# Optimization experiments

Hardware: AMD Instinct MI355X
Metric: run time of the kernel (lower is better)

The kernel has to match this reference:

```python
import jax, jax.numpy as jnp
import numpy as np

D = 2048      # hidden_size
H = 16        # num_attention_heads
KVH = 4       # num_key_value_heads
HD = 128      # head_dim
E = 32        # num_experts
TOPK = 8      # num_experts_per_tok
F = 768       # moe_intermediate_size
EPS = 1e-6
THETA = 1000000.0
B, S = 2, 1024


def setup_inputs() -> dict:
    key = jax.random.key(0)
    ks = jax.random.split(key, 16)
    sc = lambda *shape: 1.0 / np.sqrt(shape[-2] if len(shape) > 1 else shape[0])
    return {
        "hidden_states": jax.random.normal(ks[0], (B, S, D), jnp.float32),
        "attention_mask": jnp.ones((B, S), jnp.bool_),
        "input_ln_scale": jnp.ones((D,), jnp.float32),
        "post_ln_scale": jnp.ones((D,), jnp.float32),
        "q_w": jax.random.normal(ks[1], (D, H * HD), jnp.float32) * sc(D, H * HD),
        "k_w": jax.random.normal(ks[2], (D, KVH * HD), jnp.float32) * sc(D, KVH * HD),
        "v_w": jax.random.normal(ks[3], (D, KVH * HD), jnp.float32) * sc(D, KVH * HD),
        "o_w": jax.random.normal(ks[4], (H * HD, D), jnp.float32) * sc(H * HD, D),
        "q_norm_scale": jnp.ones((HD,), jnp.float32),
        "k_norm_scale": jnp.ones((HD,), jnp.float32),
        "gate_w": jax.random.normal(ks[5], (D, E), jnp.float32) * sc(D, E),
        "gate_proj": jax.random.normal(ks[6], (E, D, F), jnp.float32) * sc(E, D, F),
        "up_proj": jax.random.normal(ks[7], (E, D, F), jnp.float32) * sc(E, D, F),
        "down_proj": jax.random.normal(ks[8], (E, F, D), jnp.float32) * sc(E, F, D),
    }


def _rms(x, scale):
    return x * jax.lax.rsqrt(jnp.mean(x * x, axis=-1, keepdims=True) + EPS) * scale


def _rope(x):
    # x: [B, S, h, HD]
    half = HD // 2
    inv_freq = 1.0 / (THETA ** (jnp.arange(0, half, dtype=jnp.float32) / half))
    freqs = jnp.arange(x.shape[1], dtype=jnp.float32)[:, None] * inv_freq  # [S, HD/2]
    cos = jnp.concatenate([jnp.cos(freqs)] * 2, axis=-1)[None, :, None, :]
    sin = jnp.concatenate([jnp.sin(freqs)] * 2, axis=-1)[None, :, None, :]
    rot = jnp.concatenate([-x[..., half:], x[..., :half]], axis=-1)
    return x * cos + rot * sin


def _forward(hidden_states, attention_mask, input_ln_scale, post_ln_scale,
             q_w, k_w, v_w, o_w, q_norm_scale, k_norm_scale,
             gate_w, gate_proj, up_proj, down_proj):
    b, s, _ = hidden_states.shape
    residual = hidden_states
    h = _rms(hidden_states, input_ln_scale)

    # ---- Qwen3 attention (GQA + per-head RMSNorm + RoPE, causal) ----
    q = _rms((h @ q_w).reshape(b, s, H, HD), q_norm_scale)
    k = _rms((h @ k_w).reshape(b, s, KVH, HD), k_norm_scale)
    v = (h @ v_w).reshape(b, s, KVH, HD)
    q, k = _rope(q), _rope(k)
    rep = H // KVH
    k = jnp.repeat(k, rep, axis=2)  # [B,S,H,HD]
    v = jnp.repeat(v, rep, axis=2)
    scores = jnp.einsum('bqhd,bkhd->bhqk', q, k) * (HD ** -0.5)
    causal = jnp.tril(jnp.ones((s, s), jnp.bool_))
    mask = causal[None, None] & attention_mask[:, None, None, :]
    scores = jnp.where(mask, scores, jnp.finfo(scores.dtype).min)
    attn = jax.nn.softmax(scores, axis=-1)
    ctx = jnp.einsum('bhqk,bkhd->bqhd', attn, v).reshape(b, s, H * HD)
    h = residual + ctx @ o_w

    # ---- MoE block ----
    residual = h
    x = _rms(h, post_ln_scale).reshape(-1, D)  # [N, D]
    router_logits = x @ gate_w                 # [N, E]
    routing_weights, selected = jax.lax.top_k(router_logits, k=TOPK)
    routing_weights = jax.nn.softmax(routing_weights, axis=-1)
    sel_flat = jnp.ravel(selected)                     # [N*K]
    x_exp = jnp.repeat(x, TOPK, axis=0)                # [N*K, D]
    sort_idx = jnp.argsort(sel_flat)
    unsort_idx = jnp.argsort(sort_idx)
    x_sorted = x_exp[sort_idx]
    group_sizes = jnp.bincount(sel_flat, length=E)
    gate_out = jax.lax.ragged_dot(x_sorted, gate_proj, group_sizes)
    up_out = jax.lax.ragged_dot(x_sorted, up_proj, group_sizes)
    activated = jax.nn.silu(gate_out) * up_out
    down_out = jax.lax.ragged_dot(activated, down_proj, group_sizes)
    unsorted = down_out[unsort_idx].reshape(-1, TOPK, D)
    moe_out = (unsorted * routing_weights[..., None]).sum(axis=1).reshape(b, s, D)
    return residual + moe_out


def reference(hidden_states, attention_mask, input_ln_scale, post_ln_scale,
              q_w, k_w, v_w, o_w, q_norm_scale, k_norm_scale,
              gate_w, gate_proj, up_proj, down_proj):
    return _forward(hidden_states, attention_mask, input_ln_scale, post_ln_scale,
                    q_w, k_w, v_w, o_w, q_norm_scale, k_norm_scale,
                    gate_w, gate_proj, up_proj, down_proj)
```

## Files before the change

kernel.cpp:

```cpp
#include <hip/hip_runtime.h>
#include <hip/hip_bf16.h>

#define D_ 2048
#define H_ 16
#define KVH_ 4
#define HD_ 128
#define E_ 32
#define TOPK_ 8
#define F_ 768
#define NB_ 2
#define SS_ 1024
#define NT_ 2048
#define NPAIR_ 16384

typedef __attribute__((ext_vector_type(8))) short short8;
typedef __attribute__((ext_vector_type(4))) float floatx4;
typedef __attribute__((ext_vector_type(4))) unsigned int uintx4;
typedef __attribute__((ext_vector_type(4))) unsigned short ushortx4;

__device__ __forceinline__ unsigned short f2bf(float f) {
  union { float f; unsigned u; } v; v.f = f;
  unsigned r = v.u + 0x7FFFu + ((v.u >> 16) & 1u);
  return (unsigned short)(r >> 16);
}
__device__ __forceinline__ float bf2f(unsigned short h) {
  union { unsigned u; float f; } v; v.u = ((unsigned)h) << 16;
  return v.f;
}
__device__ __forceinline__ void split2(float v, unsigned short& hi, unsigned short& lo) {
  unsigned short h = f2bf(v);
  hi = h;
  lo = f2bf(v - bf2f(h));
}
__device__ __forceinline__ void gload16(const unsigned short* g, unsigned short* l) {
  __builtin_amdgcn_global_load_lds(
      (const __attribute__((address_space(1))) unsigned int*)g,
      (__attribute__((address_space(3))) unsigned int*)l, 16, 0, 0);
}

__global__ __launch_bounds__(256) void tconv_kernel(const float* __restrict__ src,
                                                    unsigned short* __restrict__ dst,
                                                    int R, int C) {
  size_t off = (size_t)blockIdx.z * R * C;
  src += off; dst += off;
  __shared__ float t[32][33];
  int c0 = blockIdx.x * 32, r0 = blockIdx.y * 32;
  int row = threadIdx.x >> 3, c4 = (threadIdx.x & 7) * 4;
  float4 v = *(const float4*)(src + (size_t)(r0 + row) * C + c0 + c4);
  t[row][c4 + 0] = v.x; t[row][c4 + 1] = v.y; t[row][c4 + 2] = v.z; t[row][c4 + 3] = v.w;
  __syncthreads();
  ushortx4 o = { f2bf(t[c4 + 0][row]), f2bf(t[c4 + 1][row]),
                 f2bf(t[c4 + 2][row]), f2bf(t[c4 + 3][row]) };
  *(ushortx4*)(dst + (size_t)(c0 + row) * R + r0 + c4) = o;
}

__global__ __launch_bounds__(256) void tsplit_kernel(const float* __restrict__ src,
                                                     unsigned short* __restrict__ dhi,
                                                     unsigned short* __restrict__ dlo,
                                                     int R, int C) {
  __shared__ float t[32][33];
  int c0 = blockIdx.x * 32, r0 = blockIdx.y * 32;
  int row = threadIdx.x >> 3, c4 = (threadIdx.x & 7) * 4;
  float4 v = *(const float4*)(src + (size_t)(r0 + row) * C + c0 + c4);
  t[row][c4 + 0] = v.x; t[row][c4 + 1] = v.y; t[row][c4 + 2] = v.z; t[row][c4 + 3] = v.w;
  __syncthreads();
  ushortx4 oh, ol;
  #pragma unroll
  for (int i = 0; i < 4; ++i) {
    unsigned short hi, lo;
    split2(t[c4 + i][row], hi, lo);
    oh[i] = hi; ol[i] = lo;
  }
  size_t didx = (size_t)(c0 + row) * R + r0 + c4;
  *(ushortx4*)(dhi + didx) = oh;
  *(ushortx4*)(dlo + didx) = ol;
}

template<int MODE>
__global__ __launch_bounds__(256) void rms_kernel(const float* __restrict__ in,
                                                  const float* __restrict__ sc,
                                                  float* __restrict__ outf,
                                                  unsigned short* __restrict__ o1,
                                                  unsigned short* __restrict__ o2) {
  __shared__ float red[4];
  int row = blockIdx.x, tid = threadIdx.x;
  const float4* x4 = (const float4*)(in + (size_t)row * D_);
  float4 a = x4[tid], b = x4[tid + 256];
  float ss = a.x*a.x + a.y*a.y + a.z*a.z + a.w*a.w
           + b.x*b.x + b.y*b.y + b.z*b.z + b.w*b.w;
  #pragma unroll
  for (int off = 1; off < 64; off <<= 1) ss += __shfl_xor(ss, off);
  if ((tid & 63) == 0) red[tid >> 6] = ss;
  __syncthreads();
  float r = rsqrtf((red[0] + red[1] + red[2] + red[3]) * (1.0f / D_) + 1e-6f);
  const float4* s4 = (const float4*)sc;
  float4 sa = s4[tid], sb = s4[tid + 256];
  float va[8] = { a.x*r*sa.x, a.y*r*sa.y, a.z*r*sa.z, a.w*r*sa.w,
                  b.x*r*sb.x, b.y*r*sb.y, b.z*r*sb.z, b.w*r*sb.w };
  if (MODE == 0) {
    ushortx4 h0, l0, h1, l1;
    #pragma unroll
    for (int i = 0; i < 4; ++i) { unsigned short h, l; split2(va[i], h, l); h0[i] = h; l0[i] = l; }
    #pragma unroll
    for (int i = 0; i < 4; ++i) { unsigned short h, l; split2(va[4 + i], h, l); h1[i] = h; l1[i] = l; }
    *(ushortx4*)(o1 + (size_t)row * D_ + tid * 4) = h0;
    *(ushortx4*)(o2 + (size_t)row * D_ + tid * 4) = l0;
    *(ushortx4*)(o1 + (size_t)row * D_ + 1024 + tid * 4) = h1;
    *(ushortx4*)(o2 + (size_t)row * D_ + 1024 + tid * 4) = l1;
  } else {
    *(float4*)(outf + (size_t)row * D_ + tid * 4) = make_float4(va[0], va[1], va[2], va[3]);
    *(float4*)(outf + (size_t)row * D_ + 1024 + tid * 4) = make_float4(va[4], va[5], va[6], va[7]);
    ushortx4 h0 = { f2bf(va[0]), f2bf(va[1]), f2bf(va[2]), f2bf(va[3]) };
    ushortx4 h1 = { f2bf(va[4]), f2bf(va[5]), f2bf(va[6]), f2bf(va[7]) };
    *(ushortx4*)(o1 + (size_t)row * D_ + tid * 4) = h0;
    *(ushortx4*)(o1 + (size_t)row * D_ + 1024 + tid * 4) = h1;
  }
}

template<int EPI>
__global__ __launch_bounds__(256) void gemm_bb(const unsigned short* __restrict__ Ahi,
                                               const unsigned short* __restrict__ Alo,
                                               const unsigned short* __restrict__ Bhi,
                                               const unsigned short* __restrict__ Blo,
                                               const float* __restrict__ res,
                                               float* __restrict__ out,
                                               int M, int Nn, int K) {
  __shared__ unsigned short Ah[64 * 72], Al[64 * 72], Bh[64 * 72], Bl[64 * 72];
  int tid = threadIdx.x, l = tid & 63, wid = tid >> 6;
  int lr = l & 15, lk = (l >> 4) * 8;
  int m0 = blockIdx.y * 64, n0 = blockIdx.x * 64;
  int wr = (wid >> 1) * 32, wc = (wid & 1) * 32;
  int srow = tid >> 3, sch = (tid & 7) * 8;
  size_t aoff[2], boff[2];
  int loff[2];
  #pragma unroll
  for (int i = 0; i < 2; ++i) {
    aoff[i] = (size_t)(m0 + i * 32 + srow) * K + sch;
    boff[i] = (size_t)(n0 + i * 32 + srow) * K + sch;
    loff[i] = (i * 32 + srow) * 72 + sch;
  }
  floatx4 acc[2][2];
  #pragma unroll
  for (int i = 0; i < 2; ++i)
    #pragma unroll
    for (int j = 0; j < 2; ++j) acc[i][j] = (floatx4){0.f, 0.f, 0.f, 0.f};
  for (int k0 = 0; k0 < K; k0 += 64) {
    uintx4 vah[2], val[2], vbh[2], vbl[2];
    #pragma unroll
    for (int i = 0; i < 2; ++i) {
      vah[i] = *(const uintx4*)(Ahi + aoff[i] + k0);
      val[i] = *(const uintx4*)(Alo + aoff[i] + k0);
      vbh[i] = *(const uintx4*)(Bhi + boff[i] + k0);
      vbl[i] = *(const uintx4*)(Blo + boff[i] + k0);
    }
    __syncthreads();
    #pragma unroll
    for (int i = 0; i < 2; ++i) {
      *(uintx4*)&Ah[loff[i]] = vah[i];
      *(uintx4*)&Al[loff[i]] = val[i];
      *(uintx4*)&Bh[loff[i]] = vbh[i];
      *(uintx4*)&Bl[loff[i]] = vbl[i];
    }
    __syncthreads();
    #pragma unroll
    for (int ks = 0; ks < 2; ++ks) {
      short8 ah[2], al_[2], bh[2], bl_[2];
      #pragma unroll
      for (int i = 0; i < 2; ++i) {
        ah[i]  = *(const short8*)&Ah[(wr + i * 16 + lr) * 72 + ks * 32 + lk];
        al_[i] = *(const short8*)&Al[(wr + i * 16 + lr) * 72 + ks * 32 + lk];
        bh[i]  = *(const short8*)&Bh[(wc + i * 16 + lr) * 72 + ks * 32 + lk];
        bl_[i] = *(const short8*)&Bl[(wc + i * 16 + lr) * 72 + ks * 32 + lk];
      }
      #pragma unroll
      for (int i = 0; i < 2; ++i)
        #pragma unroll
        for (int j = 0; j < 2; ++j) {
          acc[i][j] = __builtin_amdgcn_mfma_f32_16x16x32_bf16(ah[i], bh[j], acc[i][j], 0, 0, 0);
          acc[i][j] = __builtin_amdgcn_mfma_f32_16x16x32_bf16(ah[i], bl_[j], acc[i][j], 0, 0, 0);
          acc[i][j] = __builtin_amdgcn_mfma_f32_16x16x32_bf16(al_[i], bh[j], acc[i][j], 0, 0, 0);
        }
    }
  }
  int rq = (l >> 4) * 4;
  #pragma unroll
  for (int i = 0; i < 2; ++i)
    #pragma unroll
    for (int j = 0; j < 2; ++j)
      #pragma unroll
      for (int r = 0; r < 4; ++r) {
        size_t idx = (size_t)(m0 + wr + i * 16 + rq + r) * Nn + (n0 + wc + j * 16 + lr);
        float v = acc[i][j][r];
        if (EPI == 1) v += res[idx];
        out[idx] = v;
      }
}

template<int EPI>
__global__ __launch_bounds__(256) void gemm_bb128g(const unsigned short* __restrict__ Ahi,
                                                   const unsigned short* __restrict__ Alo,
                                                   const unsigned short* __restrict__ Bhi,
                                                   const unsigned short* __restrict__ Blo,
                                                   const float* __restrict__ res,
                                                   float* __restrict__ out,
                                                   int M, int Nn, int K) {
  int g = blockIdx.x;
  int nwg = gridDim.x;
  int per = nwg >> 3;
  int sw = (g & 7) * per + (g >> 3);
  int my = M >> 7;
  int xt = sw / my, yt = sw - xt * my;
  int m0 = yt * 128, n0 = xt * 128;
  __shared__ unsigned short Ah[2][128 * 32], Al[2][128 * 32];
  __shared__ unsigned short Bh[2][128 * 32], Bl[2][128 * 32];
  int tid = threadIdx.x, l = tid & 63, wid = tid >> 6;
  int lr = l & 15, lk = (l >> 4) * 8;
  int wr = (wid >> 1) * 64, wc = (wid & 1) * 64;
  int srl = l >> 2;
  int sch = ((l & 3) ^ (srl & 3)) * 8;
  size_t aoffs[2], boffs[2];
  int ldo[2];
  #pragma unroll
  for (int i = 0; i < 2; ++i) {
    int r = wid * 32 + i * 16 + srl;
    aoffs[i] = (size_t)(m0 + r) * K + sch;
    boffs[i] = (size_t)(n0 + r) * K + sch;
    ldo[i] = (wid * 32 + i * 16) * 32;
  }
  floatx4 acc[4][4];
  #pragma unroll
  for (int i = 0; i < 4; ++i)
    #pragma unroll
    for (int j = 0; j < 4; ++j) acc[i][j] = (floatx4){0.f, 0.f, 0.f, 0.f};

  auto stage = [&](int sel, int k0) {
    #pragma unroll
    for (int i = 0; i < 2; ++i) {
      gload16(Ahi + aoffs[i] + k0, &Ah[sel][ldo[i]]);
      gload16(Alo + aoffs[i] + k0, &Al[sel][ldo[i]]);
      gload16(Bhi + boffs[i] + k0, &Bh[sel][ldo[i]]);
      gload16(Blo + boffs[i] + k0, &Bl[sel][ldo[i]]);
    }
  };

  int rsw = ((l >> 4) ^ (lr & 3)) << 3;
  stage(0, 0);
  asm volatile("s_waitcnt vmcnt(0)" ::: "memory");
  __syncthreads();
  for (int k0 = 0; k0 < K; k0 += 32) {
    int cur = (k0 >> 5) & 1;
    if (k0 + 32 < K) stage(cur ^ 1, k0 + 32);
    short8 ah[4], al_[4];
    #pragma unroll
    for (int i = 0; i < 4; ++i) {
      int ao = (wr + i * 16 + lr) * 32 + rsw;
      ah[i]  = *(const short8*)&Ah[cur][ao];
      al_[i] = *(const short8*)&Al[cur][ao];
    }
    #pragma unroll
    for (int j = 0; j < 4; ++j) {
      int bo = (wc + j * 16 + lr) * 32 + rsw;
      short8 bh  = *(const short8*)&Bh[cur][bo];
      short8 bl_ = *(const short8*)&Bl[cur][bo];
      #pragma unroll
      for (int i = 0; i < 4; ++i) {
        acc[i][j] = __builtin_amdgcn_mfma_f32_16x16x32_bf16(ah[i], bh, acc[i][j], 0, 0, 0);
        acc[i][j] = __builtin_amdgcn_mfma_f32_16x16x32_bf16(ah[i], bl_, acc[i][j], 0, 0, 0);
        acc[i][j] = __builtin_amdgcn_mfma_f32_16x16x32_bf16(al_[i], bh, acc[i][j], 0, 0, 0);
      }
    }
    asm volatile("s_waitcnt vmcnt(0)" ::: "memory");
    __syncthreads();
  }
  int rq = (l >> 4) * 4;
  #pragma unroll
  for (int i = 0; i < 4; ++i)
    #pragma unroll
    for (int j = 0; j < 4; ++j)
      #pragma unroll
      for (int r = 0; r < 4; ++r) {
        size_t idx = (size_t)(m0 + wr + i * 16 + rq + r) * Nn + (n0 + wc + j * 16 + lr);
        float v = acc[i][j][r];
        if (EPI == 1) v += res[idx];
        out[idx] = v;
      }
}

__global__ __launch_bounds__(256) void qknorm_rope_kernel(const float* __restrict__ qb,
                                                          const float* __restrict__ kb,
                                                          const float* __restrict__ qs,
                                                          const float* __restrict__ ks,
                                                          unsigned short* __restrict__ qhi,
                                                          unsigned short* __restrict__ qlo,
                                                          unsigned short* __restrict__ khi,
                                                          unsigned short* __restrict__ klo) {
  int gw = blockIdx.x * 4 + (threadIdx.x >> 6);
  int l = threadIdx.x & 63;
  const float* ptr; const float* sc; unsigned short *dhi, *dlo; int t;
  size_t orow;
  if (gw < NT_ * H_) { ptr = qb + (size_t)gw * HD_; sc = qs; dhi = qhi; dlo = qlo; orow = (size_t)gw * HD_; t = gw >> 4; }
  else { int r = gw - NT_ * H_; ptr = kb + (size_t)r * HD_; sc = ks; dhi = khi; dlo = klo; orow = (size_t)r * HD_; t = r >> 2; }
  int pos = t & (SS_ - 1);
  float2 x = *(const float2*)(ptr + 2 * l);
  float p2 = x.x * x.x + x.y * x.y;
  #pragma unroll
  for (int off = 1; off < 64; off <<= 1) p2 += __shfl_xor(p2, off);
  float rms = rsqrtf(p2 * (1.0f / HD_) + 1e-6f);
  float nx = x.x * rms * sc[2 * l];
  float ny = x.y * rms * sc[2 * l + 1];
  int j0 = (2 * l) & 63;
  float ang0 = pos * __expf(-(float)j0 * (13.815510557964274f / 64.0f));
  float ang1 = pos * __expf(-(float)(j0 + 1) * (13.815510557964274f / 64.0f));
  float s0, c0, s1, c1;
  sincosf(ang0, &s0, &c0);
  sincosf(ang1, &s1, &c1);
  float ox = __shfl_xor(nx, 32);
  float oy = __shfl_xor(ny, 32);
  float r0, r1;
  if (l < 32) { r0 = nx * c0 - ox * s0; r1 = ny * c1 - oy * s1; }
  else        { r0 = nx * c0 + ox * s0; r1 = ny * c1 + oy * s1; }
  unsigned short h0, l0, h1, l1;
  split2(r0, h0, l0);
  split2(r1, h1, l1);
  *(unsigned*)(dhi + orow + 2 * l) = (unsigned)h0 | ((unsigned)h1 << 16);
  *(unsigned*)(dlo + orow + 2 * l) = (unsigned)l0 | ((unsigned)l1 << 16);
}

__global__ __launch_bounds__(256) void vsplit_kernel(const float* __restrict__ vbuf,
                                                     unsigned short* __restrict__ vthi,
                                                     unsigned short* __restrict__ vtlo) {
  int d0 = blockIdx.x * 32, s0 = blockIdx.y * 32, bk = blockIdx.z;
  int b = bk >> 2, kvh = bk & 3;
  __shared__ float t[32][33];
  int row = threadIdx.x >> 3, c4 = (threadIdx.x & 7) * 4;
  float4 v = *(const float4*)(vbuf + ((size_t)(b * SS_ + s0 + row) * KVH_ + kvh) * HD_ + d0 + c4);
  t[row][c4 + 0] = v.x; t[row][c4 + 1] = v.y; t[row][c4 + 2] = v.z; t[row][c4 + 3] = v.w;
  __syncthreads();
  ushortx4 oh, ol;
  #pragma unroll
  for (int i = 0; i < 4; ++i) {
    unsigned short hi, lo;
    split2(t[c4 + i][row], hi, lo);
    oh[i] = hi; ol[i] = lo;
  }
  size_t idx = ((size_t)(b * KVH_ + kvh) * HD_ + d0 + row) * SS_ + s0 + c4;
  *(ushortx4*)(vthi + idx) = oh;
  *(ushortx4*)(vtlo + idx) = ol;
}

__global__ __launch_bounds__(256) void attn_kernel(const unsigned short* __restrict__ qhi,
                                                   const unsigned short* __restrict__ qlo,
                                                   const unsigned short* __restrict__ khi,
                                                   const unsigned short* __restrict__ klo,
                                                   const unsigned short* __restrict__ vthi,
                                                   const unsigned short* __restrict__ vtlo,
                                                   unsigned short* __restrict__ ctx_hi,
                                                   unsigned short* __restrict__ ctx_lo) {
  int qt = blockIdx.x, h = blockIdx.y, b = blockIdx.z;
  int kvh = h >> 2;
  int tid = threadIdx.x, l = tid & 63, wid = tid >> 6;
  int lr = l & 15, lk = (l >> 4) * 8;
  __shared__ unsigned short Kh[2][32 * 128], Kl[2][32 * 128];
  __shared__ unsigned short Vh[2][128 * 32], Vl[2][128 * 32];
  __shared__ unsigned short Ph[64 * 40], Pl[64 * 40];
  int qt0 = qt * 64;

  size_t qrow = ((size_t)((b * SS_ + qt0 + wid * 16 + lr) * H_) + h) * HD_;
  short8 qfh[4], qfl[4];
  #pragma unroll
  for (int t = 0; t < 4; ++t) {
    qfh[t] = *(const short8*)(qhi + qrow + t * 32 + lk);
    qfl[t] = *(const short8*)(qlo + qrow + t * 32 + lk);
  }

  float m[4], sum[4];
  #pragma unroll
  for (int r = 0; r < 4; ++r) { m[r] = -__builtin_inff(); sum[r] = 0.f; }
  floatx4 o[8];
  #pragma unroll
  for (int cb = 0; cb < 8; ++cb) o[cb] = (floatx4){0.f, 0.f, 0.f, 0.f};

  size_t vbase = ((size_t)(b * KVH_ + kvh) * HD_) * SS_;
  int nt = 2 * qt + 2;

  auto stage = [&](int sel, int kt) {
    int k0 = kt * 32;
    #pragma unroll
    for (int i = 0; i < 2; ++i) {
      int r = wid * 8 + i * 4 + (l >> 4);
      int ch = (l & 15) ^ (r & 7);
      size_t gk = ((size_t)((b * SS_ + k0 + r) * KVH_) + kvh) * HD_ + ch * 8;
      gload16(khi + gk, &Kh[sel][(wid * 8 + i * 4) * 128]);
      gload16(klo + gk, &Kl[sel][(wid * 8 + i * 4) * 128]);
    }
    #pragma unroll
    for (int i = 0; i < 2; ++i) {
      int r = wid * 32 + i * 16 + (l >> 2);
      int ch = (l & 3) ^ (r & 3);
      size_t gv = vbase + (size_t)r * SS_ + k0 + ch * 8;
      gload16(vthi + gv, &Vh[sel][(wid * 32 + i * 16) * 32]);
      gload16(vtlo + gv, &Vl[sel][(wid * 32 + i * 16) * 32]);
    }
  };

  stage(0, 0);
  asm volatile("s_waitcnt vmcnt(0)" ::: "memory");
  __syncthreads();

  for (int kt = 0; kt < nt; ++kt) {
    int cur = kt & 1;
    if (kt + 1 < nt) stage(cur ^ 1, kt + 1);
    int k0 = kt * 32;
    float sv[2][4];
    #pragma unroll
    for (int kbk = 0; kbk < 2; ++kbk) {
      int kr = kbk * 16 + lr;
      floatx4 s = (floatx4){0.f, 0.f, 0.f, 0.f};
      #pragma unroll
      for (int t = 0; t < 4; ++t) {
        int co = kr * 128 + (((t * 4 + (l >> 4)) ^ (lr & 7)) << 3);
        short8 kfh = *(const short8*)&Kh[cur][co];
        short8 kfl = *(const short8*)&Kl[cur][co];
        s = __builtin_amdgcn_mfma_f32_16x16x32_bf16(qfh[t], kfh, s, 0, 0, 0);
        s = __builtin_amdgcn_mfma_f32_16x16x32_bf16(qfh[t], kfl, s, 0, 0, 0);
        s = __builtin_amdgcn_mfma_f32_16x16x32_bf16(qfl[t], kfh, s, 0, 0, 0);
      }
      int key = k0 + kr;
      #pragma unroll
      for (int r = 0; r < 4; ++r) {
        int q = qt0 + wid * 16 + (l >> 4) * 4 + r;
        float x = s[r] * 0.08838834764831845f;
        sv[kbk][r] = (key <= q) ? x : -1e30f;
      }
    }
    float f[4], p[2][4];
    #pragma unroll
    for (int r = 0; r < 4; ++r) {
      float tm = fmaxf(sv[0][r], sv[1][r]);
      tm = fmaxf(tm, __shfl_xor(tm, 1));
      tm = fmaxf(tm, __shfl_xor(tm, 2));
      tm = fmaxf(tm, __shfl_xor(tm, 4));
      tm = fmaxf(tm, __shfl_xor(tm, 8));
      float mn = fmaxf(m[r], tm);
      f[r] = __expf(m[r] - mn);
      m[r] = mn;
      float rs = 0.f;
      #pragma unroll
      for (int kbk = 0; kbk < 2; ++kbk) { p[kbk][r] = __expf(sv[kbk][r] - mn); rs += p[kbk][r]; }
      rs += __shfl_xor(rs, 1); rs += __shfl_xor(rs, 2);
      rs += __shfl_xor(rs, 4); rs += __shfl_xor(rs, 8);
      sum[r] = sum[r] * f[r] + rs;
    }
    #pragma unroll
    for (int kbk = 0; kbk < 2; ++kbk)
      #pragma unroll
      for (int r = 0; r < 4; ++r)
        split2(p[kbk][r],
               Ph[(wid * 16 + (l >> 4) * 4 + r) * 40 + kbk * 16 + lr],
               Pl[(wid * 16 + (l >> 4) * 4 + r) * 40 + kbk * 16 + lr]);
    #pragma unroll
    for (int cb = 0; cb < 8; ++cb)
      #pragma unroll
      for (int r = 0; r < 4; ++r) o[cb][r] = o[cb][r] * f[r];
    int pco = (wid * 16 + lr) * 40 + lk;
    short8 pah = *(const short8*)&Ph[pco];
    short8 pal = *(const short8*)&Pl[pco];
    #pragma unroll
    for (int cb = 0; cb < 8; ++cb) {
      int vo = (cb * 16 + lr) * 32 + (((l >> 4) ^ (lr & 3)) << 3);
      short8 vbh = *(const short8*)&Vh[cur][vo];
      short8 vbl = *(const short8*)&Vl[cur][vo];
      o[cb] = __builtin_amdgcn_mfma_f32_16x16x32_bf16(pah, vbh, o[cb], 0, 0, 0);
      o[cb] = __builtin_amdgcn_mfma_f32_16x16x32_bf16(pah, vbl, o[cb], 0, 0, 0);
      o[cb] = __builtin_amdgcn_mfma_f32_16x16x32_bf16(pal, vbh, o[cb], 0, 0, 0);
    }
    asm volatile("s_waitcnt vmcnt(0)" ::: "memory");
    __syncthreads();
  }
  #pragma unroll
  for (int cb = 0; cb < 8; ++cb)
    #pragma unroll
    for (int r = 0; r < 4; ++r) {
      int q = qt0 + wid * 16 + (l >> 4) * 4 + r;
      int d = cb * 16 + lr;
      float val = o[cb][r] / sum[r];
      unsigned short hi, lo;
      split2(val, hi, lo);
      size_t idx = ((size_t)(b * SS_ + q)) * (H_ * HD_) + h * HD_ + d;
      ctx_hi[idx] = hi;
      ctx_lo[idx] = lo;
    }
}

__global__ __launch_bounds__(256) void router_kernel(const float* __restrict__ x2,
                                                     const float* __restrict__ gw,
                                                     float* __restrict__ logits) {
  int t = blockIdx.x * 4 + (threadIdx.x >> 6);
  int l = threadIdx.x & 63;
  float acc[32];
  #pragma unroll
  for (int e = 0; e < 32; ++e) acc[e] = 0.f;
  for (int i = 0; i < 32; ++i) {
    int d = i * 64 + l;
    float xv = x2[(size_t)t * D_ + d];
    const float4* wr = (const float4*)(gw + (size_t)d * E_);
    #pragma unroll
    for (int j = 0; j < 8; ++j) {
      float4 wv = wr[j];
      acc[4 * j + 0] += xv * wv.x; acc[4 * j + 1] += xv * wv.y;
      acc[4 * j + 2] += xv * wv.z; acc[4 * j + 3] += xv * wv.w;
    }
  }
  #pragma unroll
  for (int e = 0; e < 32; ++e) {
    acc[e] += __shfl_xor(acc[e], 1);  acc[e] += __shfl_xor(acc[e], 2);
    acc[e] += __shfl_xor(acc[e], 4);  acc[e] += __shfl_xor(acc[e], 8);
    acc[e] += __shfl_xor(acc[e], 16); acc[e] += __shfl_xor(acc[e], 32);
  }
  if (l == 0) {
    #pragma unroll
    for (int e = 0; e < 32; ++e) logits[(size_t)t * E_ + e] = acc[e];
  }
}

__global__ void topk_kernel(const float* __restrict__ logits, int* __restrict__ sel,
                            float* __restrict__ wts, int* __restrict__ counts) {
  int t = blockIdx.x * blockDim.x + threadIdx.x;
  if (t >= NT_) return;
  float v[32];
  for (int e = 0; e < 32; ++e) v[e] = logits[(size_t)t * E_ + e];
  float val[8]; int idx[8];
  for (int k = 0; k < 8; ++k) {
    float best = -__builtin_inff(); int bi = 0;
    for (int e = 0; e < 32; ++e) if (v[e] > best) { best = v[e]; bi = e; }
    val[k] = best; idx[k] = bi; v[bi] = -__builtin_inff();
  }
  float mx = val[0], s = 0.f; float ex[8];
  for (int k = 0; k < 8; ++k) { ex[k] = expf(val[k] - mx); s += ex[k]; }
  float inv = 1.f / s;
  for (int k = 0; k < 8; ++k) {
    sel[t * 8 + k] = idx[k];
    wts[t * 8 + k] = ex[k] * inv;
    atomicAdd(&counts[idx[k]], 1);
  }
}

__global__ void scan_kernel(const int* __restrict__ counts, int* __restrict__ offs,
                            int* __restrict__ cursors) {
  if (threadIdx.x == 0) {
    int c = 0;
    for (int e = 0; e < E_; ++e) { offs[e] = c; cursors[e] = c; c += counts[e]; }
  }
}

__global__ void scatter_kernel(const int* __restrict__ sel, const float* __restrict__ wts,
                               int* __restrict__ cursors, int* __restrict__ pair_t,
                               float* __restrict__ pair_w, int* __restrict__ pos) {
  int g = blockIdx.x * blockDim.x + threadIdx.x;
  if (g >= NPAIR_) return;
  int e = sel[g];
  int p = atomicAdd(&cursors[e], 1);
  pair_t[p] = g >> 3;
  pair_w[p] = wts[g];
  pos[g] = p;
}

__global__ __launch_bounds__(256, 4) void gateup_kernel(const unsigned short* __restrict__ xbf,
                                                        const unsigned short* __restrict__ gT,
                                                        const unsigned short* __restrict__ uT,
                                                        const int* __restrict__ counts,
                                                        const int* __restrict__ offs,
                                                        const int* __restrict__ pair_t,
                                                        const float* __restrict__ pair_w,
                                                        unsigned short* __restrict__ act) {
  int g = blockIdx.x;
  int lg = (g & ~127) | (((g & 7) << 4) | ((g >> 3) & 15));
  int e = lg / 192;
  int rem = lg - e * 192;
  int xt = rem >> 4, yt = rem & 15;
  int cnt = counts[e];
  int r0 = yt * 128;
  if (r0 >= cnt) return;
  int base = offs[e];
  int n0 = xt * 64;
  const unsigned short* G = gT + (size_t)e * F_ * D_;
  const unsigned short* U = uT + (size_t)e * F_ * D_;
  __shared__ unsigned short As[2][128 * 32], Gs[2][64 * 32], Us[2][64 * 32];
  int tid = threadIdx.x, l = tid & 63, wid = tid >> 6;
  int lr = l & 15, lk16 = l >> 4;
  int srl = l >> 2;
  int sch = ((l & 3) ^ ((srl >> 1) & 3)) * 8;
  const unsigned short* asrc[2];
  #pragma unroll
  for (int i = 0; i < 2; ++i) {
    int rowt = wid * 32 + i * 16 + srl;
    int cr = r0 + rowt; if (cr > cnt - 1) cr = cnt - 1;
    asrc[i] = xbf + (size_t)pair_t[base + cr] * D_ + sch;
  }
  const unsigned short* gsrc = G + (size_t)(n0 + wid * 16 + srl) * D_ + sch;
  const unsigned short* usrc = U + (size_t)(n0 + wid * 16 + srl) * D_ + sch;
  int wm = wid >> 1;
  int wn = wid & 1;
  floatx4 ag[4][2], au[4][2];
  #pragma unroll
  for (int i = 0; i < 4; ++i)
    #pragma unroll
    for (int j = 0; j < 2; ++j) { ag[i][j] = (floatx4){0.f,0.f,0.f,0.f}; au[i][j] = (floatx4){0.f,0.f,0.f,0.f}; }

  auto stage = [&](int sel, int kofs) {
    gload16(asrc[0] + kofs, &As[sel][(wid * 32) * 32]);
    gload16(asrc[1] + kofs, &As[sel][(wid * 32 + 16) * 32]);
    gload16(gsrc + kofs, &Gs[sel][(wid * 16) * 32]);
    gload16(usrc + kofs, &Us[sel][(wid * 16) * 32]);
  };

  stage(0, 0);
  asm volatile("s_waitcnt vmcnt(0)" ::: "memory");
  __syncthreads();
  const int nt = D_ / 32;
  for (int t = 0; t < nt; ++t) {
    int cur = t & 1;
    if (t + 1 < nt) stage(cur ^ 1, (t + 1) * 32);
    int co = (lk16 ^ ((lr >> 1) & 3)) << 3;
    short8 a[4], gg[2], uu[2];
    #pragma unroll
    for (int i = 0; i < 4; ++i)
      a[i] = *(const short8*)&As[cur][(wm * 64 + i * 16 + lr) * 32 + co];
    #pragma unroll
    for (int j = 0; j < 2; ++j) {
      gg[j] = *(const short8*)&Gs[cur][(wn * 32 + j * 16 + lr) * 32 + co];
      uu[j] = *(const short8*)&Us[cur][(wn * 32 + j * 16 + lr) * 32 + co];
    }
    #pragma unroll
    for (int i = 0; i < 4; ++i)
      #pragma unroll
      for (int j = 0; j < 2; ++j) {
        ag[i][j] = __builtin_amdgcn_mfma_f32_16x16x32_bf16(a[i], gg[j], ag[i][j], 0, 0, 0);
        au[i][j] = __builtin_amdgcn_mfma_f32_16x16x32_bf16(a[i], uu[j], au[i][j], 0, 0, 0);
      }
    asm volatile("s_waitcnt vmcnt(0)" ::: "memory");
    __syncthreads();
  }
  int rq = (l >> 4) * 4;
  #pragma unroll
  for (int i = 0; i < 4; ++i)
    #pragma unroll
    for (int r = 0; r < 4; ++r) {
      int rowl = wm * 64 + i * 16 + rq + r;
      if (r0 + rowl < cnt) {
        int p = base + r0 + rowl;
        float pw = pair_w[p];
        size_t orow = (size_t)p * F_;
        #pragma unroll
        for (int j = 0; j < 2; ++j) {
          float gv = ag[i][j][r], uv = au[i][j][r];
          float a = (gv / (1.f + __expf(-gv))) * uv * pw;
          act[orow + n0 + wn * 32 + j * 16 + lr] = f2bf(a);
        }
      }
    }
}

__global__ __launch_bounds__(256, 4) void down_kernel(const unsigned short* __restrict__ act,
                                                      const unsigned short* __restrict__ dT,
                                                      const int* __restrict__ counts,
                                                      const int* __restrict__ offs,
                                                      float* __restrict__ dpre) {
  int g = blockIdx.x;
  int lg = (g & ~255) | (((g & 7) << 5) | ((g >> 3) & 31));
  int e = lg >> 8;
  int rem = lg & 255;
  int xt = rem >> 4, yt = rem & 15;
  int cnt = counts[e];
  int r0 = yt * 128;
  if (r0 >= cnt) return;
  int base = offs[e];
  int n0 = xt * 128;
  const unsigned short* B = dT + (size_t)e * ((size_t)D_ * F_);
  __shared__ unsigned short As[2][128 * 32], Bs[2][128 * 32];
  int tid = threadIdx.x, l = tid & 63, wid = tid >> 6;
  int lr = l & 15, lk16 = l >> 4;
  int srl = l >> 2;
  int sch = ((l & 3) ^ ((srl >> 1) & 3)) * 8;
  const unsigned short* asrc[2];
  const unsigned short* bsrc[2];
  #pragma unroll
  for (int i = 0; i < 2; ++i) {
    int rowt = wid * 32 + i * 16 + srl;
    int cr = r0 + rowt; if (cr > cnt - 1) cr = cnt - 1;
    asrc[i] = act + (size_t)(base + cr) * F_ + sch;
    bsrc[i] = B + (size_t)(n0 + rowt) * F_ + sch;
  }
  int wm = wid >> 1;
  int wn = wid & 1;
  floatx4 acc[4][4];
  #pragma unroll
  for (int i = 0; i < 4; ++i)
    #pragma unroll
    for (int j = 0; j < 4; ++j) acc[i][j] = (floatx4){0.f, 0.f, 0.f, 0.f};

  auto stage = [&](int sel, int kofs) {
    gload16(asrc[0] + kofs, &As[sel][(wid * 32) * 32]);
    gload16(asrc[1] + kofs, &As[sel][(wid * 32 + 16) * 32]);
    gload16(bsrc[0] + kofs, &Bs[sel][(wid * 32) * 32]);
    gload16(bsrc[1] + kofs, &Bs[sel][(wid * 32 + 16) * 32]);
  };

  stage(0, 0);
  asm volatile("s_waitcnt vmcnt(0)" ::: "memory");
  __syncthreads();
  const int nt = F_ / 32;
  for (int t = 0; t < nt; ++t) {
    int cur = t & 1;
    if (t + 1 < nt) stage(cur ^ 1, (t + 1) * 32);
    int co = (lk16 ^ ((lr >> 1) & 3)) << 3;
    short8 a[4], b_[4];
    #pragma unroll
    for (int i = 0; i < 4; ++i) {
      a[i]  = *(const short8*)&As[cur][(wm * 64 + i * 16 + lr) * 32 + co];
      b_[i] = *(const short8*)&Bs[cur][(wn * 64 + i * 16 + lr) * 32 + co];
    }
    #pragma unroll
    for (int i = 0; i < 4; ++i)
      #pragma unroll
      for (int j = 0; j < 4; ++j)
        acc[i][j] = __builtin_amdgcn_mfma_f32_16x16x32_bf16(a[i], b_[j], acc[i][j], 0, 0, 0);
    asm volatile("s_waitcnt vmcnt(0)" ::: "memory");
    __syncthreads();
  }
  int rq = (l >> 4) * 4;
  #pragma unroll
  for (int i = 0; i < 4; ++i)
    #pragma unroll
    for (int r = 0; r < 4; ++r) {
      int rowl = wm * 64 + i * 16 + rq + r;
      if (r0 + rowl < cnt) {
        size_t orow = (size_t)(base + r0 + rowl) * D_;
        #pragma unroll
        for (int j = 0; j < 4; ++j)
          dpre[orow + n0 + wn * 64 + j * 16 + lr] = acc[i][j][r];
      }
    }
}

__global__ __launch_bounds__(256) void moe_gather_kernel(const float* __restrict__ dpre,
                                                         const int* __restrict__ pos,
                                                         float* __restrict__ out) {
  int t = blockIdx.x;
  int tid = threadIdx.x;
  int p[8];
  #pragma unroll
  for (int k = 0; k < 8; ++k) p[k] = pos[t * 8 + k];
  size_t orow = (size_t)t * D_;
  #pragma unroll
  for (int j = 0; j < 2; ++j) {
    int col = tid * 4 + j * 1024;
    float4 s = *(const float4*)(out + orow + col);
    #pragma unroll
    for (int k = 0; k < 8; ++k) {
      float4 v = *(const float4*)(dpre + (size_t)p[k] * D_ + col);
      s.x += v.x; s.y += v.y; s.z += v.z; s.w += v.w;
    }
    *(float4*)(out + orow + col) = s;
  }
}

extern "C" void kernel_launch(void* const* d_in, const int* in_sizes, int n_in,
                              void* d_out, int out_size, void* d_ws, size_t ws_size,
                              hipStream_t stream) {
  const float* hidden  = (const float*)d_in[0];
  const float* in_ln   = (const float*)d_in[2];
  const float* post_ln = (const float*)d_in[3];
  const float* q_w     = (const float*)d_in[4];
  const float* k_w     = (const float*)d_in[5];
  const float* v_w     = (const float*)d_in[6];
  const float* o_w     = (const float*)d_in[7];
  const float* q_ns    = (const float*)d_in[8];
  const float* k_ns    = (const float*)d_in[9];
  const float* gate_w  = (const float*)d_in[10];
  const float* gate_p  = (const float*)d_in[11];
  const float* up_p    = (const float*)d_in[12];
  const float* down_p  = (const float*)d_in[13];
  float* out = (float*)d_out;

  char* w = (char*)d_ws;
  size_t off = 0;
  auto alloc = [&](size_t b) { char* p = w + off; off += (b + 255) & ~(size_t)255; return p; };
  unsigned short* qThi = (unsigned short*)alloc((size_t)2048 * 2048 * 2);
  unsigned short* qTlo = (unsigned short*)alloc((size_t)2048 * 2048 * 2);
  unsigned short* kThi = (unsigned short*)alloc((size_t)512 * 2048 * 2);
  unsigned short* kTlo = (unsigned short*)alloc((size_t)512 * 2048 * 2);
  unsigned short* vThi = (unsigned short*)alloc((size_t)512 * 2048 * 2);
  unsigned short* vTlo = (unsigned short*)alloc((size_t)512 * 2048 * 2);
  unsigned short* oThi = (unsigned short*)alloc((size_t)2048 * 2048 * 2);
  unsigned short* oTlo = (unsigned short*)alloc((size_t)2048 * 2048 * 2);
  unsigned short* gT   = (unsigned short*)alloc((size_t)E_ * F_ * D_ * 2);
  unsigned short* uT   = (unsigned short*)alloc((size_t)E_ * F_ * D_ * 2);
  unsigned short* dT   = (unsigned short*)alloc((size_t)E_ * D_ * F_ * 2);
  unsigned short* h_hi = (unsigned short*)alloc((size_t)NT_ * D_ * 2);
  unsigned short* h_lo = (unsigned short*)alloc((size_t)NT_ * D_ * 2);
  float* qbuf  = (float*)alloc((size_t)NT_ * H_ * HD_ * 4);
  float* kbuf  = (float*)alloc((size_t)NT_ * KVH_ * HD_ * 4);
  float* vbuf  = (float*)alloc((size_t)NT_ * KVH_ * HD_ * 4);
  unsigned short* qhi = (unsigned short*)alloc((size_t)NT_ * H_ * HD_ * 2);
  unsigned short* qlo = (unsigned short*)alloc((size_t)NT_ * H_ * HD_ * 2);
  unsigned short* khi = (unsigned short*)alloc((size_t)NT_ * KVH_ * HD_ * 2);
  unsigned short* klo = (unsigned short*)alloc((size_t)NT_ * KVH_ * HD_ * 2);
  unsigned short* vthi = (unsigned short*)alloc((size_t)NT_ * KVH_ * HD_ * 2);
  unsigned short* vtlo = (unsigned short*)alloc((size_t)NT_ * KVH_ * HD_ * 2);
  unsigned short* ctx_hi = (unsigned short*)alloc((size_t)NT_ * H_ * HD_ * 2);
  unsigned short* ctx_lo = (unsigned short*)alloc((size_t)NT_ * H_ * HD_ * 2);
  float* x2    = (float*)alloc((size_t)NT_ * D_ * 4);
  unsigned short* x2bf = (unsigned short*)alloc((size_t)NT_ * D_ * 2);
  float* logits = (float*)alloc((size_t)NT_ * E_ * 4);
  int*   sel    = (int*)alloc((size_t)NT_ * TOPK_ * 4);
  float* wts    = (float*)alloc((size_t)NT_ * TOPK_ * 4);
  int*   counts = (int*)alloc(E_ * 4);
  int*   offs   = (int*)alloc(E_ * 4);
  int*   curs   = (int*)alloc(E_ * 4);
  int*   pair_t = (int*)alloc((size_t)NPAIR_ * 4);
  float* pair_w = (float*)alloc((size_t)NPAIR_ * 4);
  int*   pos    = (int*)alloc((size_t)NPAIR_ * 4);
  unsigned short* act = (unsigned short*)alloc((size_t)NPAIR_ * F_ * 2);
  float* dpre  = (float*)alloc((size_t)NPAIR_ * D_ * 4);

  tsplit_kernel<<<dim3(64, 64), 256, 0, stream>>>(q_w, qThi, qTlo, 2048, 2048);
  tsplit_kernel<<<dim3(16, 64), 256, 0, stream>>>(k_w, kThi, kTlo, 2048, 512);
  tsplit_kernel<<<dim3(16, 64), 256, 0, stream>>>(v_w, vThi, vTlo, 2048, 512);
  tsplit_kernel<<<dim3(64, 64), 256, 0, stream>>>(o_w, oThi, oTlo, 2048, 2048);
  tconv_kernel<<<dim3(24, 64, 32), 256, 0, stream>>>(gate_p, gT, 2048, 768);
  tconv_kernel<<<dim3(24, 64, 32), 256, 0, stream>>>(up_p, uT, 2048, 768);
  tconv_kernel<<<dim3(64, 24, 32), 256, 0, stream>>>(down_p, dT, 768, 2048);

  rms_kernel<0><<<NT_, 256, 0, stream>>>(hidden, in_ln, nullptr, h_hi, h_lo);
  gemm_bb128g<0><<<256, 256, 0, stream>>>(h_hi, h_lo, qThi, qTlo, nullptr, qbuf, NT_, 2048, 2048);
  gemm_bb<0><<<dim3(8, 32), 256, 0, stream>>>(h_hi, h_lo, kThi, kTlo, nullptr, kbuf, NT_, 512, 2048);
  gemm_bb<0><<<dim3(8, 32), 256, 0, stream>>>(h_hi, h_lo, vThi, vTlo, nullptr, vbuf, NT_, 512, 2048);
  qknorm_rope_kernel<<<(NT_ * (H_ + KVH_)) / 4, 256, 0, stream>>>(qbuf, kbuf, q_ns, k_ns,
                                                                  qhi, qlo, khi, klo);
  vsplit_kernel<<<dim3(HD_ / 32, SS_ / 32, NB_ * KVH_), 256, 0, stream>>>(vbuf, vthi, vtlo);
  attn_kernel<<<dim3(SS_ / 64, H_, NB_), 256, 0, stream>>>(qhi, qlo, khi, klo, vthi, vtlo,
                                                           ctx_hi, ctx_lo);
  gemm_bb128g<1><<<256, 256, 0, stream>>>(ctx_hi, ctx_lo, oThi, oTlo, hidden, out, NT_, 2048, 2048);
  rms_kernel<1><<<NT_, 256, 0, stream>>>(out, post_ln, x2, x2bf, nullptr);
  (void)hipMemsetAsync(counts, 0, E_ * 4, stream);
  router_kernel<<<NT_ / 4, 256, 0, stream>>>(x2, gate_w, logits);
  topk_kernel<<<NT_ / 256, 256, 0, stream>>>(logits, sel, wts, counts);
  scan_kernel<<<1, 64, 0, stream>>>(counts, offs, curs);
  scatter_kernel<<<NPAIR_ / 256, 256, 0, stream>>>(sel, wts, curs, pair_t, pair_w, pos);
  gateup_kernel<<<192 * 32, 256, 0, stream>>>(x2bf, gT, uT, counts, offs, pair_t, pair_w, act);
  down_kernel<<<256 * 32, 256, 0, stream>>>(act, dT, counts, offs, dpre);
  moe_gather_kernel<<<NT_, 256, 0, stream>>>(dpre, pos, out);
}
```

Baseline: 1.046 ms.

## Triple-buffer MoE GEMM pipelines and store down-projection output as bf16

```diff
diff --git a/kernel.cpp b/kernel.cpp
--- a/kernel.cpp
+++ b/kernel.cpp
@@ -565,7 +565,7 @@
   pos[g] = p;
 }
 
-__global__ __launch_bounds__(256, 4) void gateup_kernel(const unsigned short* __restrict__ xbf,
+__global__ __launch_bounds__(256, 3) void gateup_kernel(const unsigned short* __restrict__ xbf,
                                                         const unsigned short* __restrict__ gT,
                                                         const unsigned short* __restrict__ uT,
                                                         const int* __restrict__ counts,
@@ -585,7 +585,7 @@
   int n0 = xt * 64;
   const unsigned short* G = gT + (size_t)e * F_ * D_;
   const unsigned short* U = uT + (size_t)e * F_ * D_;
-  __shared__ unsigned short As[2][128 * 32], Gs[2][64 * 32], Us[2][64 * 32];
+  __shared__ unsigned short As[3][128 * 32], Gs[3][64 * 32], Us[3][64 * 32];
   int tid = threadIdx.x, l = tid & 63, wid = tid >> 6;
   int lr = l & 15, lk16 = l >> 4;
   int srl = l >> 2;
@@ -614,13 +614,16 @@
     gload16(usrc + kofs, &Us[sel][(wid * 16) * 32]);
   };
 
+  const int nt = D_ / 32;
   stage(0, 0);
-  asm volatile("s_waitcnt vmcnt(0)" ::: "memory");
-  __syncthreads();
-  const int nt = D_ / 32;
+  stage(1, 32);
   for (int t = 0; t < nt; ++t) {
-    int cur = t & 1;
-    if (t + 1 < nt) stage(cur ^ 1, (t + 1) * 32);
+    int cur = t % 3;
+    if (t + 1 < nt) { asm volatile("s_waitcnt vmcnt(4)" ::: "memory"); }
+    else            { asm volatile("s_waitcnt vmcnt(0)" ::: "memory"); }
+    __builtin_amdgcn_sched_barrier(0);
+    __syncthreads();
+    if (t + 2 < nt) stage((t + 2) % 3, (t + 2) * 32);
     int co = (lk16 ^ ((lr >> 1) & 3)) << 3;
     short8 a[4], gg[2], uu[2];
     #pragma unroll
@@ -631,6 +634,7 @@
       gg[j] = *(const short8*)&Gs[cur][(wn * 32 + j * 16 + lr) * 32 + co];
       uu[j] = *(const short8*)&Us[cur][(wn * 32 + j * 16 + lr) * 32 + co];
     }
+    __builtin_amdgcn_s_setprio(1);
     #pragma unroll
     for (int i = 0; i < 4; ++i)
       #pragma unroll
@@ -638,8 +642,7 @@
         ag[i][j] = __builtin_amdgcn_mfma_f32_16x16x32_bf16(a[i], gg[j], ag[i][j], 0, 0, 0);
         au[i][j] = __builtin_amdgcn_mfma_f32_16x16x32_bf16(a[i], uu[j], au[i][j], 0, 0, 0);
       }
-    asm volatile("s_waitcnt vmcnt(0)" ::: "memory");
-    __syncthreads();
+    __builtin_amdgcn_s_setprio(0);
   }
   int rq = (l >> 4) * 4;
   #pragma unroll
@@ -661,11 +664,11 @@
     }
 }
 
-__global__ __launch_bounds__(256, 4) void down_kernel(const unsigned short* __restrict__ act,
+__global__ __launch_bounds__(256, 3) void down_kernel(const unsigned short* __restrict__ act,
                                                       const unsigned short* __restrict__ dT,
                                                       const int* __restrict__ counts,
                                                       const int* __restrict__ offs,
-                                                      float* __restrict__ dpre) {
+                                                      unsigned short* __restrict__ dpre) {
   int g = blockIdx.x;
   int lg = (g & ~255) | (((g & 7) << 5) | ((g >> 3) & 31));
   int e = lg >> 8;
@@ -677,7 +680,7 @@
   int base = offs[e];
   int n0 = xt * 128;
   const unsigned short* B = dT + (size_t)e * ((size_t)D_ * F_);
-  __shared__ unsigned short As[2][128 * 32], Bs[2][128 * 32];
+  __shared__ unsigned short As[3][128 * 32], Bs[3][128 * 32];
   int tid = threadIdx.x, l = tid & 63, wid = tid >> 6;
   int lr = l & 15, lk16 = l >> 4;
   int srl = l >> 2;
@@ -706,13 +709,16 @@
     gload16(bsrc[1] + kofs, &Bs[sel][(wid * 32 + 16) * 32]);
   };
 
+  const int nt = F_ / 32;
   stage(0, 0);
-  asm volatile("s_waitcnt vmcnt(0)" ::: "memory");
-  __syncthreads();
-  const int nt = F_ / 32;
+  stage(1, 32);
   for (int t = 0; t < nt; ++t) {
-    int cur = t & 1;
-    if (t + 1 < nt) stage(cur ^ 1, (t + 1) * 32);
+    int cur = t % 3;
+    if (t + 1 < nt) { asm volatile("s_waitcnt vmcnt(4)" ::: "memory"); }
+    else            { asm volatile("s_waitcnt vmcnt(0)" ::: "memory"); }
+    __builtin_amdgcn_sched_barrier(0);
+    __syncthreads();
+    if (t + 2 < nt) stage((t + 2) % 3, (t + 2) * 32);
     int co = (lk16 ^ ((lr >> 1) & 3)) << 3;
     short8 a[4], b_[4];
     #pragma unroll
@@ -720,13 +726,13 @@
       a[i]  = *(const short8*)&As[cur][(wm * 64 + i * 16 + lr) * 32 + co];
       b_[i] = *(const short8*)&Bs[cur][(wn * 64 + i * 16 + lr) * 32 + co];
     }
+    __builtin_amdgcn_s_setprio(1);
     #pragma unroll
     for (int i = 0; i < 4; ++i)
       #pragma unroll
       for (int j = 0; j < 4; ++j)
         acc[i][j] = __builtin_amdgcn_mfma_f32_16x16x32_bf16(a[i], b_[j], acc[i][j], 0, 0, 0);
-    asm volatile("s_waitcnt vmcnt(0)" ::: "memory");
-    __syncthreads();
+    __builtin_amdgcn_s_setprio(0);
   }
   int rq = (l >> 4) * 4;
   #pragma unroll
@@ -738,12 +744,12 @@
         size_t orow = (size_t)(base + r0 + rowl) * D_;
         #pragma unroll
         for (int j = 0; j < 4; ++j)
-          dpre[orow + n0 + wn * 64 + j * 16 + lr] = acc[i][j][r];
+          dpre[orow + n0 + wn * 64 + j * 16 + lr] = f2bf(acc[i][j][r]);
       }
     }
 }
 
-__global__ __launch_bounds__(256) void moe_gather_kernel(const float* __restrict__ dpre,
+__global__ __launch_bounds__(256) void moe_gather_kernel(const unsigned short* __restrict__ dpre,
                                                          const int* __restrict__ pos,
                                                          float* __restrict__ out) {
   int t = blockIdx.x;
@@ -752,17 +758,20 @@
   #pragma unroll
   for (int k = 0; k < 8; ++k) p[k] = pos[t * 8 + k];
   size_t orow = (size_t)t * D_;
-  #pragma unroll
-  for (int j = 0; j < 2; ++j) {
-    int col = tid * 4 + j * 1024;
-    float4 s = *(const float4*)(out + orow + col);
-    #pragma unroll
-    for (int k = 0; k < 8; ++k) {
-      float4 v = *(const float4*)(dpre + (size_t)p[k] * D_ + col);
-      s.x += v.x; s.y += v.y; s.z += v.z; s.w += v.w;
-    }
-    *(float4*)(out + orow + col) = s;
-  }
+  int col = tid * 8;
+  float s[8];
+  float4 o0 = *(const float4*)(out + orow + col);
+  float4 o1 = *(const float4*)(out + orow + col + 4);
+  s[0] = o0.x; s[1] = o0.y; s[2] = o0.z; s[3] = o0.w;
+  s[4] = o1.x; s[5] = o1.y; s[6] = o1.z; s[7] = o1.w;
+  #pragma unroll
+  for (int k = 0; k < 8; ++k) {
+    short8 v = *(const short8*)(dpre + (size_t)p[k] * D_ + col);
+    #pragma unroll
+    for (int j = 0; j < 8; ++j) s[j] += bf2f((unsigned short)v[j]);
+  }
+  *(float4*)(out + orow + col) = make_float4(s[0], s[1], s[2], s[3]);
+  *(float4*)(out + orow + col + 4) = make_float4(s[4], s[5], s[6], s[7]);
 }
 
 extern "C" void kernel_launch(void* const* d_in, const int* in_sizes, int n_in,
@@ -822,7 +831,7 @@
   float* pair_w = (float*)alloc((size_t)NPAIR_ * 4);
   int*   pos    = (int*)alloc((size_t)NPAIR_ * 4);
   unsigned short* act = (unsigned short*)alloc((size_t)NPAIR_ * F_ * 2);
-  float* dpre  = (float*)alloc((size_t)NPAIR_ * D_ * 4);
+  unsigned short* dpre = (unsigned short*)alloc((size_t)NPAIR_ * D_ * 2);
 
   tsplit_kernel<<<dim3(64, 64), 256, 0, stream>>>(q_w, qThi, qTlo, 2048, 2048);
   tsplit_kernel<<<dim3(16, 64), 256, 0, stream>>>(k_w, kThi, kTlo, 2048, 512);
```

Measured after the change: 1.024 ms (median of 2 runs). 1.02x faster.
